# Performance work log

Measured on AMD Instinct MI355X. Metric: run time of the kernel, lower is better.

## Reference

```python
import math
import jax, jax.numpy as jnp
import numpy as np

DIM = 1024
HID = 2048  # dim * expansion_factor
QK = 128
G = 256  # group size
NUM_BUCKETS = 32
MAX_DIST = 128
SCALE = QK ** 0.5


def t5_rel_bias(rel_emb, g):
    # non-causal T5 relative position bias over a g x g window
    pos = jnp.arange(g)
    n = pos[:, None] - pos[None, :]  # n = -(k - q) = q - k
    nb = NUM_BUCKETS // 2  # 16
    ret = (n < 0).astype(jnp.int32) * nb
    n = jnp.abs(n)
    max_exact = nb // 2  # 8
    is_small = n < max_exact
    val_large = max_exact + (
        jnp.log(jnp.maximum(n, 1).astype(jnp.float32) / max_exact)
        / math.log(MAX_DIST / max_exact) * (nb - max_exact)
    ).astype(jnp.int32)
    val_large = jnp.minimum(val_large, nb - 1)
    bucket = ret + jnp.where(is_small, n, val_large)
    return rel_emb[bucket, 0] * SCALE  # [g, g]


def setup_inputs() -> dict:
    key = jax.random.key(0)
    ks = jax.random.split(key, 8)
    d = {}
    d['x'] = jax.random.normal(ks[0], (4, 4096, DIM), dtype=jnp.float32)
    d['ln_g'] = jnp.ones((DIM,), jnp.float32)
    d['ln_b'] = jnp.zeros((DIM,), jnp.float32)
    d['W_h'] = jax.random.normal(ks[1], (DIM, 2 * HID), jnp.float32) * (1.0 / math.sqrt(DIM))
    d['b_h'] = jnp.zeros((2 * HID,), jnp.float32)
    d['W_qk'] = jax.random.normal(ks[2], (DIM, QK), jnp.float32) * (1.0 / math.sqrt(DIM))
    d['b_qk'] = jnp.zeros((QK,), jnp.float32)
    d['os_g'] = 1.0 + 0.02 * jax.random.normal(ks[3], (4, QK), jnp.float32)
    d['os_b'] = jnp.zeros((4, QK), jnp.float32)
    d['rel_emb'] = jax.random.normal(ks[4], (NUM_BUCKETS, 1), jnp.float32)
    d['W_o'] = jax.random.normal(ks[5], (HID, DIM), jnp.float32) * (1.0 / math.sqrt(HID))
    d['b_o'] = jnp.zeros((DIM,), jnp.float32)
    return d


def reference(x, ln_g, ln_b, W_h, b_h, W_qk, b_qk, os_g, os_b, rel_emb, W_o, b_o):
    b, n, _ = x.shape
    # LayerNorm
    mu = jnp.mean(x, axis=-1, keepdims=True)
    var = jnp.var(x, axis=-1, keepdims=True)
    normed = (x - mu) * jax.lax.rsqrt(var + 1e-5) * ln_g + ln_b
    # to_hidden -> v, gate ; to_qk
    hidden = jax.nn.silu(normed @ W_h + b_h)  # [b, n, 2*HID]
    v, gate = hidden[..., :HID], hidden[..., HID:]
    qk = jax.nn.silu(normed @ W_qk + b_qk)  # [b, n, QK]
    # offset-scale into 4 heads
    heads = qk[..., None, :] * os_g + os_b  # [b, n, 4, QK]
    quad_q, lin_q, quad_k, lin_k = [heads[..., h, :] for h in range(4)]
    # group: n divisible by G (no padding needed)
    ng = n // G
    grp = lambda t: t.reshape(b, ng, G, -1)
    quad_q, quad_k, lin_q, lin_k, vg = map(grp, (quad_q, quad_k, lin_q, lin_k, v))
    # grouped quadratic attention with ReLU^2 and T5 bias
    sim = jnp.einsum('bgid,bgjd->bgij', quad_q, quad_k) / G
    sim = sim + t5_rel_bias(rel_emb, G)
    attn = jnp.square(jax.nn.relu(sim))
    quad_out = jnp.einsum('bgij,bgjd->bgid', attn, vg)
    # linear attention, reduced over groups (non-causal)
    lin_kv = jnp.einsum('bgnd,bgne->bde', lin_k, vg) / n
    lin_out = jnp.einsum('bgnd,bde->bgne', lin_q, lin_kv)
    out = gate * (quad_out.reshape(b, n, HID) + lin_out.reshape(b, n, HID))
    return out @ W_o + b_o + x
```

## Files before the change

### kernel.cpp

```cpp
#include <hip/hip_runtime.h>
#include <hip/hip_bf16.h>

typedef float  f32x4  __attribute__((ext_vector_type(4)));
typedef __bf16 bf16x8 __attribute__((ext_vector_type(8)));
typedef __bf16 bf16x4 __attribute__((ext_vector_type(4)));

__device__ __forceinline__ float silu_f(float x) { return x / (1.0f + __expf(-x)); }

__device__ __forceinline__ void gload16(const __bf16* g, const char* lds) {
    __builtin_amdgcn_global_load_lds((const __attribute__((address_space(1))) void*)g,
                                     (__attribute__((address_space(3))) void*)lds, 16, 0, 0);
}

__global__ __launch_bounds__(256) void ln_kernel(const float* __restrict__ x,
                                                 const float* __restrict__ g,
                                                 const float* __restrict__ b,
                                                 __bf16* __restrict__ out) {
    int row = blockIdx.x;
    const float* xr = x + (long)row * 1024;
    int t = threadIdx.x;
    f32x4 v = *(const f32x4*)(xr + t * 4);
    float s  = v[0] + v[1] + v[2] + v[3];
    float ss = v[0]*v[0] + v[1]*v[1] + v[2]*v[2] + v[3]*v[3];
    #pragma unroll
    for (int off = 32; off > 0; off >>= 1) {
        s  += __shfl_down(s, off);
        ss += __shfl_down(ss, off);
    }
    __shared__ float red[8];
    int wave = t >> 6, lane = t & 63;
    if (lane == 0) { red[wave*2] = s; red[wave*2+1] = ss; }
    __syncthreads();
    float S  = red[0] + red[2] + red[4] + red[6];
    float SS = red[1] + red[3] + red[5] + red[7];
    float mean = S * (1.0f/1024.0f);
    float var  = SS * (1.0f/1024.0f) - mean*mean;
    float rstd = rsqrtf(var + 1e-5f);
    __bf16* orow = out + (long)row * 1024;
    #pragma unroll
    for (int j = 0; j < 4; j++) {
        float fv = (v[j] - mean) * rstd * g[t*4+j] + b[t*4+j];
        orow[t*4+j] = (__bf16)fv;
    }
}

__global__ __launch_bounds__(256) void prep_kernel(const float* __restrict__ W_h,
                                                   const float* __restrict__ W_qk,
                                                   const float* __restrict__ W_o,
                                                   const float* __restrict__ rel_emb,
                                                   __bf16* __restrict__ WhT,
                                                   __bf16* __restrict__ WqkT,
                                                   __bf16* __restrict__ WoT,
                                                   float* __restrict__ bmat) {
    __shared__ __bf16 tile[32][33];
    int id = blockIdx.x, tid = threadIdx.x;
    if (id >= 6272) {
        int idx = (id - 6272) * 256 + tid;
        int i = idx >> 8, j = idx & 255;
        int n = i - j;
        int ret = (n < 0) ? 16 : 0;
        int an = (n < 0) ? -n : n;
        int bucket;
        if (an < 8) {
            bucket = ret + an;
        } else {
            float vl = logf((float)an * 0.125f) / 2.772588722239781f * 8.0f;
            int lv = 8 + (int)vl;
            bucket = ret + (lv < 15 ? lv : 15);
        }
        bmat[idx] = rel_emb[bucket] * 11.313708498984761f;
        return;
    }
    const float* in; __bf16* outp; int rows, cols, tx, ty;
    if (id < 4096)      { in = W_h;  outp = WhT;  rows = 1024; cols = 4096; tx = id % 128; ty = id / 128; }
    else if (id < 4224) { int t = id - 4096; in = W_qk; outp = WqkT; rows = 1024; cols = 128;  tx = t % 4;  ty = t / 4; }
    else                { int t = id - 4224; in = W_o;  outp = WoT;  rows = 2048; cols = 1024; tx = t % 32; ty = t / 32; }
    int c0 = tx * 32, r0 = ty * 32;
    int lx = tid & 31, ly = tid >> 5;
    #pragma unroll
    for (int i = 0; i < 4; i++) {
        int r = ly + i*8;
        tile[r][lx] = (__bf16)in[(long)(r0 + r) * cols + c0 + lx];
    }
    __syncthreads();
    #pragma unroll
    for (int i = 0; i < 4; i++) {
        int c = ly + i*8;
        outp[(long)(c0 + c) * rows + r0 + lx] = tile[lx][c];
    }
}

__global__ __launch_bounds__(256) void reduce8_kernel(const __bf16* __restrict__ in,
                                                      __bf16* __restrict__ out) {
    int i = (blockIdx.x * 256 + threadIdx.x) * 4;
    int b = i >> 18;
    int r = i & 262143;
    float s0 = 0.f, s1 = 0.f, s2 = 0.f, s3 = 0.f;
    #pragma unroll
    for (int c = 0; c < 8; ++c) {
        bf16x4 v = *(const bf16x4*)(in + ((long)(b*8 + c) << 18) + r);
        s0 += (float)v[0]; s1 += (float)v[1]; s2 += (float)v[2]; s3 += (float)v[3];
    }
    bf16x4 o; o[0] = (__bf16)s0; o[1] = (__bf16)s1; o[2] = (__bf16)s2; o[3] = (__bf16)s3;
    *(bf16x4*)(out + i) = o;
}

struct GP {
    const __bf16* A;
    const __bf16* B;
    const __bf16* A2;
    const __bf16* B2;
    int lda, ldb, kSteps;
    long sAz, sBz, sCz;
    float scale;
    float* outF;
    __bf16 *o0, *o1, *o2, *o3;
    const float *c0, *c1, *c2;
    __bf16* gbuf;
};

template<int EPI>
__global__ __launch_bounds__(256, 2) void gemm64_kernel(GP p) {
    __shared__ __bf16 As[2*128*32];
    __shared__ __bf16 Bs[2*128*32];
    const __bf16* A = p.A + (long)blockIdx.x * 128 * p.lda;
    const __bf16* B = p.B + (long)blockIdx.y * 128 * p.ldb;
    int tid = threadIdx.x;
    int wave = tid >> 6, lane = tid & 63;
    int wr = (wave >> 1) * 64, wc = (wave & 1) * 64;
    int lr = lane & 15, kg = lane >> 4;

    f32x4 acc[4][4] = {};

    int lsub = lane >> 2;
    int scol = (lane & 3) * 8;
    const __bf16* Ag = A + scol + (long)(wave*32 + lsub) * p.lda;
    const __bf16* Bg = B + scol + (long)(wave*32 + lsub) * p.ldb;
    long a16 = (long)16 * p.lda, b16 = (long)16 * p.ldb;
    __bf16* AsW = As + wave * 32 * 32;
    __bf16* BsW = Bs + wave * 32 * 32;

    for (int ks = 0; ks < p.kSteps; ++ks) {
        long k0 = (long)ks * 64;
        __syncthreads();
        gload16(Ag + k0,            (const char*)AsW);
        gload16(Ag + k0 + a16,      (const char*)(AsW + 16*32));
        gload16(Bg + k0,            (const char*)BsW);
        gload16(Bg + k0 + b16,      (const char*)(BsW + 16*32));
        gload16(Ag + k0 + 32,       (const char*)(AsW + 4096));
        gload16(Ag + k0 + 32 + a16, (const char*)(AsW + 4096 + 16*32));
        gload16(Bg + k0 + 32,       (const char*)(BsW + 4096));
        gload16(Bg + k0 + 32 + b16, (const char*)(BsW + 4096 + 16*32));
        __syncthreads();
#pragma unroll
        for (int kk = 0; kk < 2; ++kk) {
            bf16x8 af[4], bfr[4];
            #pragma unroll
            for (int i = 0; i < 4; i++) af[i]  = *(const bf16x8*)(As + kk*4096 + (wr + i*16 + lr)*32 + kg*8);
            #pragma unroll
            for (int i = 0; i < 4; i++) bfr[i] = *(const bf16x8*)(Bs + kk*4096 + (wc + i*16 + lr)*32 + kg*8);
            #pragma unroll
            for (int i = 0; i < 4; i++)
                #pragma unroll
                for (int j = 0; j < 4; j++)
                    acc[i][j] = __builtin_amdgcn_mfma_f32_16x16x32_bf16(af[i], bfr[j], acc[i][j], 0, 0, 0);
        }
    }

    int bx = blockIdx.x, by = blockIdx.y;
    #pragma unroll
    for (int i = 0; i < 4; i++) {
        #pragma unroll
        for (int j = 0; j < 4; j++) {
            int row0 = bx*128 + wr + i*16 + kg*4;
            int col  = by*128 + wc + j*16 + lr;
            if constexpr (EPI == 0) {
                if (col < 2048) {
                    bf16x4 vv;
                    #pragma unroll
                    for (int q = 0; q < 4; q++) vv[q] = (__bf16)silu_f(acc[i][j][q] + p.c0[col]);
                    *(bf16x4*)(p.o0 + (long)col*16384 + row0) = vv;
                } else {
                    #pragma unroll
                    for (int q = 0; q < 4; q++)
                        p.o1[(long)(row0+q)*2048 + (col - 2048)] = (__bf16)silu_f(acc[i][j][q] + p.c0[col]);
                }
            } else {
                #pragma unroll
                for (int q = 0; q < 4; q++) {
                    long idx = (long)(row0+q)*1024 + col;
                    p.outF[idx] = acc[i][j][q] + p.c0[col] + p.c1[idx];
                }
            }
        }
    }
}

template<int EPI>
__global__ __launch_bounds__(256, 2) void gemm_kernel(GP p) {
    __shared__ __bf16 As[128*32];
    __shared__ __bf16 Bs[128*32];
    int z = blockIdx.z;
    const __bf16* A = p.A + (long)z * p.sAz + (long)blockIdx.x * 128 * p.lda;
    const __bf16* B = p.B + (long)z * p.sBz + (long)blockIdx.y * 128 * p.ldb;
    int tid = threadIdx.x;
    int wave = tid >> 6, lane = tid & 63;
    int wr = (wave >> 1) * 64, wc = (wave & 1) * 64;
    int lr = lane & 15, kg = lane >> 4;

    f32x4 acc[4][4] = {};

    int lsub = lane >> 2;
    int scol = (lane & 3) * 8;
    const __bf16* Ag = A + scol + (long)(wave*32 + lsub) * p.lda;
    const __bf16* Bg = B + scol + (long)(wave*32 + lsub) * p.ldb;
    long a16 = (long)16 * p.lda, b16 = (long)16 * p.ldb;
    __bf16* AsW = As + wave * 32 * 32;
    __bf16* BsW = Bs + wave * 32 * 32;

    for (int ks = 0; ks < p.kSteps; ++ks) {
        long k0 = (long)ks * 32;
        __syncthreads();
        gload16(Ag + k0,       (const char*)AsW);
        gload16(Ag + k0 + a16, (const char*)(AsW + 16*32));
        gload16(Bg + k0,       (const char*)BsW);
        gload16(Bg + k0 + b16, (const char*)(BsW + 16*32));
        __syncthreads();
        bf16x8 af[4], bfr[4];
        #pragma unroll
        for (int i = 0; i < 4; i++) af[i]  = *(const bf16x8*)(As + (wr + i*16 + lr)*32 + kg*8);
        #pragma unroll
        for (int i = 0; i < 4; i++) bfr[i] = *(const bf16x8*)(Bs + (wc + i*16 + lr)*32 + kg*8);
        #pragma unroll
        for (int i = 0; i < 4; i++)
            #pragma unroll
            for (int j = 0; j < 4; j++)
                acc[i][j] = __builtin_amdgcn_mfma_f32_16x16x32_bf16(af[i], bfr[j], acc[i][j], 0, 0, 0);
    }

    int bx = blockIdx.x, by = blockIdx.y;
    #pragma unroll
    for (int i = 0; i < 4; i++) {
        #pragma unroll
        for (int j = 0; j < 4; j++) {
            int row0 = bx*128 + wr + i*16 + kg*4;
            int col  = by*128 + wc + j*16 + lr;
            if constexpr (EPI == 1) {
                float sv[4];
                #pragma unroll
                for (int q = 0; q < 4; q++) sv[q] = silu_f(acc[i][j][q] + p.c0[col]);
                #pragma unroll
                for (int q = 0; q < 4; q++) {
                    p.o0[(long)(row0+q)*128 + col] = (__bf16)(sv[q] * p.c1[      col] + p.c2[      col]);
                    p.o1[(long)(row0+q)*128 + col] = (__bf16)(sv[q] * p.c1[256 + col] + p.c2[256 + col]);
                    p.o2[(long)(row0+q)*128 + col] = (__bf16)(sv[q] * p.c1[128 + col] + p.c2[128 + col]);
                }
                bf16x4 lk;
                #pragma unroll
                for (int q = 0; q < 4; q++) lk[q] = (__bf16)(sv[q] * p.c1[384 + col] + p.c2[384 + col]);
                *(bf16x4*)(p.o3 + (long)col*16384 + row0) = lk;
            }
        }
    }
}

__global__ __launch_bounds__(256, 2) void simlinkv_kernel(GP ps, GP pl) {
    __shared__ __bf16 As[128*32];
    __shared__ __bf16 Bs[128*32];
    int id = blockIdx.x;
    bool sim = id < 256;
    GP p = sim ? ps : pl;
    int bx, by, z;
    if (sim) { bx = id & 1; by = (id >> 1) & 1; z = id >> 2; }
    else     { int t = id - 256; bx = 0; by = t & 15; z = t >> 4; }

    const __bf16* A = p.A + (long)z * p.sAz + (long)bx * 128 * p.lda;
    const __bf16* B = p.B + (long)z * p.sBz + (long)by * 128 * p.ldb;
    int tid = threadIdx.x;
    int wave = tid >> 6, lane = tid & 63;
    int wr = (wave >> 1) * 64, wc = (wave & 1) * 64;
    int lr = lane & 15, kg = lane >> 4;

    f32x4 acc[4][4] = {};

    int lsub = lane >> 2;
    int scol = (lane & 3) * 8;
    const __bf16* Ag = A + scol + (long)(wave*32 + lsub) * p.lda;
    const __bf16* Bg = B + scol + (long)(wave*32 + lsub) * p.ldb;
    long a16 = (long)16 * p.lda, b16 = (long)16 * p.ldb;
    __bf16* AsW = As + wave * 32 * 32;
    __bf16* BsW = Bs + wave * 32 * 32;

    for (int ks = 0; ks < p.kSteps; ++ks) {
        long k0 = (long)ks * 32;
        __syncthreads();
        gload16(Ag + k0,       (const char*)AsW);
        gload16(Ag + k0 + a16, (const char*)(AsW + 16*32));
        gload16(Bg + k0,       (const char*)BsW);
        gload16(Bg + k0 + b16, (const char*)(BsW + 16*32));
        __syncthreads();
        bf16x8 af[4], bfr[4];
        #pragma unroll
        for (int i = 0; i < 4; i++) af[i]  = *(const bf16x8*)(As + (wr + i*16 + lr)*32 + kg*8);
        #pragma unroll
        for (int i = 0; i < 4; i++) bfr[i] = *(const bf16x8*)(Bs + (wc + i*16 + lr)*32 + kg*8);
        #pragma unroll
        for (int i = 0; i < 4; i++)
            #pragma unroll
            for (int j = 0; j < 4; j++)
                acc[i][j] = __builtin_amdgcn_mfma_f32_16x16x32_bf16(af[i], bfr[j], acc[i][j], 0, 0, 0);
    }

    #pragma unroll
    for (int i = 0; i < 4; i++) {
        #pragma unroll
        for (int j = 0; j < 4; j++) {
            int row0 = bx*128 + wr + i*16 + kg*4;
            int col  = by*128 + wc + j*16 + lr;
            if (sim) {
                #pragma unroll
                for (int q = 0; q < 4; q++) {
                    int row = row0 + q;
                    float s = acc[i][j][q] * (1.0f/256.0f) + p.c0[row*256 + col];
                    s = fmaxf(s, 0.0f);
                    p.o0[(long)z*p.sCz + (long)row*256 + col] = (__bf16)(s * s);
                }
            } else {
                bf16x4 vv;
                #pragma unroll
                for (int q = 0; q < 4; q++) vv[q] = (__bf16)(acc[i][j][q] * p.scale);
                *(bf16x4*)(p.o0 + (long)z*p.sCz + (long)col*128 + row0) = vv;
            }
        }
    }
}

__global__ __launch_bounds__(256, 2) void quadlin_kernel(GP p) {
    __shared__ __bf16 As[128*32];
    __shared__ __bf16 Bs[128*32];
    int z = blockIdx.z;
    int batch = z >> 4;
    int tid = threadIdx.x;
    int wave = tid >> 6, lane = tid & 63;
    int wr = (wave >> 1) * 64, wc = (wave & 1) * 64;
    int lr = lane & 15, kg = lane >> 4;
    int lsub = lane >> 2;
    int scol = (lane & 3) * 8;
    __bf16* AsW = As + wave * 32 * 32;
    __bf16* BsW = Bs + wave * 32 * 32;

    f32x4 acc[4][4] = {};

    {
        const __bf16* Ag = p.A + (long)z * 65536 + (long)blockIdx.x * 128 * 256
                         + scol + (long)(wave*32 + lsub) * 256;
        const __bf16* Bg = p.B + (long)z * 256 + (long)blockIdx.y * 128 * 16384
                         + scol + (long)(wave*32 + lsub) * 16384;
        for (int ks = 0; ks < 8; ++ks) {
            long k0 = (long)ks * 32;
            __syncthreads();
            gload16(Ag + k0,             (const char*)AsW);
            gload16(Ag + k0 + 16*256,    (const char*)(AsW + 16*32));
            gload16(Bg + k0,             (const char*)BsW);
            gload16(Bg + k0 + 16L*16384, (const char*)(BsW + 16*32));
            __syncthreads();
            bf16x8 af[4], bfr[4];
            #pragma unroll
            for (int i = 0; i < 4; i++) af[i]  = *(const bf16x8*)(As + (wr + i*16 + lr)*32 + kg*8);
            #pragma unroll
            for (int i = 0; i < 4; i++) bfr[i] = *(const bf16x8*)(Bs + (wc + i*16 + lr)*32 + kg*8);
            #pragma unroll
            for (int i = 0; i < 4; i++)
                #pragma unroll
                for (int j = 0; j < 4; j++)
                    acc[i][j] = __builtin_amdgcn_mfma_f32_16x16x32_bf16(af[i], bfr[j], acc[i][j], 0, 0, 0);
        }
    }
    {
        const __bf16* Ag = p.A2 + ((long)z * 256 + (long)blockIdx.x * 128) * 128
                         + scol + (long)(wave*32 + lsub) * 128;
        const __bf16* Bg = p.B2 + (long)batch * 2048 * 128 + (long)blockIdx.y * 128 * 128
                         + scol + (long)(wave*32 + lsub) * 128;
        for (int ks = 0; ks < 4; ++ks) {
            long k0 = (long)ks * 32;
            __syncthreads();
            gload16(Ag + k0,          (const char*)AsW);
            gload16(Ag + k0 + 16*128, (const char*)(AsW + 16*32));
            gload16(Bg + k0,          (const char*)BsW);
            gload16(Bg + k0 + 16*128, (const char*)(BsW + 16*32));
            __syncthreads();
            bf16x8 af[4], bfr[4];
            #pragma unroll
            for (int i = 0; i < 4; i++) af[i]  = *(const bf16x8*)(As + (wr + i*16 + lr)*32 + kg*8);
            #pragma unroll
            for (int i = 0; i < 4; i++) bfr[i] = *(const bf16x8*)(Bs + (wc + i*16 + lr)*32 + kg*8);
            #pragma unroll
            for (int i = 0; i < 4; i++)
                #pragma unroll
                for (int j = 0; j < 4; j++)
                    acc[i][j] = __builtin_amdgcn_mfma_f32_16x16x32_bf16(af[i], bfr[j], acc[i][j], 0, 0, 0);
        }
    }
    #pragma unroll
    for (int i = 0; i < 4; i++) {
        #pragma unroll
        for (int j = 0; j < 4; j++) {
            int row0 = z*256 + blockIdx.x*128 + wr + i*16 + kg*4;
            int col  = blockIdx.y*128 + wc + j*16 + lr;
            #pragma unroll
            for (int q = 0; q < 4; q++) {
                long idx = (long)(row0+q)*2048 + col;
                float g = (float)p.gbuf[idx];
                p.gbuf[idx] = (__bf16)(g * acc[i][j][q]);
            }
        }
    }
}

extern "C" void kernel_launch(void* const* d_in, const int* in_sizes, int n_in,
                              void* d_out, int out_size, void* d_ws, size_t ws_size,
                              hipStream_t stream) {
    const float* x       = (const float*)d_in[0];
    const float* ln_g    = (const float*)d_in[1];
    const float* ln_b    = (const float*)d_in[2];
    const float* W_h     = (const float*)d_in[3];
    const float* b_h     = (const float*)d_in[4];
    const float* W_qk    = (const float*)d_in[5];
    const float* b_qk    = (const float*)d_in[6];
    const float* os_g    = (const float*)d_in[7];
    const float* os_b    = (const float*)d_in[8];
    const float* rel_emb = (const float*)d_in[9];
    const float* W_o     = (const float*)d_in[10];
    const float* b_o     = (const float*)d_in[11];
    float* out = (float*)d_out;

    const size_t MB = 1024 * 1024;
    if (ws_size < 190 * MB) return;

    char* ws = (char*)d_ws;
    __bf16* gate = (__bf16*)(ws + 0);
    __bf16* vT   = (__bf16*)(ws + 64*MB);
    __bf16* norm = (__bf16*)(ws + 128*MB);
    __bf16* attn = (__bf16*)(ws + 128*MB);
    __bf16* lkvT = (__bf16*)(ws + 136*MB);
    __bf16* lkvP = (__bf16*)(ws + 140*MB);
    __bf16* qq   = (__bf16*)(ws + 160*MB);
    __bf16* qk2  = (__bf16*)(ws + 164*MB);
    __bf16* lq   = (__bf16*)(ws + 168*MB);
    __bf16* lkT  = (__bf16*)(ws + 172*MB);
    float*  bmat = (float* )(ws + 176*MB);
    __bf16* WqkT = (__bf16*)(ws + 176*MB + 256*1024);
    __bf16* WoT  = (__bf16*)(ws + 177*MB);
    __bf16* WhT  = (__bf16*)(ws + 181*MB);

    prep_kernel<<<6528, 256, 0, stream>>>(W_h, W_qk, W_o, rel_emb, WhT, WqkT, WoT, bmat);
    ln_kernel<<<16384, 256, 0, stream>>>(x, ln_g, ln_b, norm);

    {
        GP p{}; p.A = norm; p.B = WhT; p.lda = 1024; p.ldb = 1024; p.kSteps = 16;
        p.c0 = b_h; p.o0 = vT; p.o1 = gate;
        gemm64_kernel<0><<<dim3(128, 32), 256, 0, stream>>>(p);
    }
    {
        GP p{}; p.A = norm; p.B = WqkT; p.lda = 1024; p.ldb = 1024; p.kSteps = 32;
        p.c0 = b_qk; p.c1 = os_g; p.c2 = os_b;
        p.o0 = qq; p.o1 = qk2; p.o2 = lq; p.o3 = lkT;
        gemm_kernel<1><<<dim3(128, 1, 1), 256, 0, stream>>>(p);
    }
    {
        GP ps{}; ps.A = qq; ps.B = qk2; ps.lda = 128; ps.ldb = 128; ps.kSteps = 4;
        ps.sAz = 256*128; ps.sBz = 256*128; ps.sCz = 256*256;
        ps.c0 = bmat; ps.o0 = attn;
        GP pl{}; pl.A = lkT; pl.B = vT; pl.lda = 16384; pl.ldb = 16384; pl.kSteps = 16;
        pl.sAz = 512; pl.sBz = 512; pl.sCz = 2048*128; pl.scale = 1.0f/4096.0f;
        pl.o0 = lkvP;
        simlinkv_kernel<<<768, 256, 0, stream>>>(ps, pl);
    }
    reduce8_kernel<<<1024, 256, 0, stream>>>(lkvP, lkvT);
    {
        GP p{}; p.A = attn; p.B = vT; p.A2 = lq; p.B2 = lkvT; p.gbuf = gate;
        quadlin_kernel<<<dim3(2, 16, 64), 256, 0, stream>>>(p);
    }
    {
        GP p{}; p.A = gate; p.B = WoT; p.lda = 2048; p.ldb = 2048; p.kSteps = 32;
        p.c0 = b_o; p.c1 = x; p.outF = out;
        gemm64_kernel<6><<<dim3(128, 8), 256, 0, stream>>>(p);
    }
}
```

Baseline: 433.6 us.

## Fuse prep with layernorm, merge qk GEMM into hidden GEMM, use K=64 steps

Merges the weight-prep and layernorm launches into one kernel by block-index ranges. The small qk projection, previously a 128-block GEMM, becomes an extra column tile (by==32) of the hidden-projection GEMM, so it runs alongside the big GEMM instead of as a separate underfilled launch. The sim/linkv and quad/lin kernels now load 64-wide K slices per barrier pair, halving the number of sync iterations at the cost of doubled LDS per block. Together these aim to cut launch count, tail underutilization and barrier overhead.

```diff
diff --git a/kernel.cpp b/kernel.cpp
--- a/kernel.cpp
+++ b/kernel.cpp
@@ -12,48 +12,48 @@
                                      (__attribute__((address_space(3))) void*)lds, 16, 0, 0);
 }
 
-__global__ __launch_bounds__(256) void ln_kernel(const float* __restrict__ x,
-                                                 const float* __restrict__ g,
-                                                 const float* __restrict__ b,
-                                                 __bf16* __restrict__ out) {
-    int row = blockIdx.x;
-    const float* xr = x + (long)row * 1024;
-    int t = threadIdx.x;
-    f32x4 v = *(const f32x4*)(xr + t * 4);
-    float s  = v[0] + v[1] + v[2] + v[3];
-    float ss = v[0]*v[0] + v[1]*v[1] + v[2]*v[2] + v[3]*v[3];
-    #pragma unroll
-    for (int off = 32; off > 0; off >>= 1) {
-        s  += __shfl_down(s, off);
-        ss += __shfl_down(ss, off);
-    }
+__global__ __launch_bounds__(256) void prepln_kernel(const float* __restrict__ x,
+                                                     const float* __restrict__ ln_g,
+                                                     const float* __restrict__ ln_b,
+                                                     __bf16* __restrict__ norm,
+                                                     const float* __restrict__ W_h,
+                                                     const float* __restrict__ W_qk,
+                                                     const float* __restrict__ W_o,
+                                                     const float* __restrict__ rel_emb,
+                                                     __bf16* __restrict__ WhT,
+                                                     __bf16* __restrict__ WqkT,
+                                                     __bf16* __restrict__ WoT,
+                                                     float* __restrict__ bmat) {
     __shared__ float red[8];
-    int wave = t >> 6, lane = t & 63;
-    if (lane == 0) { red[wave*2] = s; red[wave*2+1] = ss; }
-    __syncthreads();
-    float S  = red[0] + red[2] + red[4] + red[6];
-    float SS = red[1] + red[3] + red[5] + red[7];
-    float mean = S * (1.0f/1024.0f);
-    float var  = SS * (1.0f/1024.0f) - mean*mean;
-    float rstd = rsqrtf(var + 1e-5f);
-    __bf16* orow = out + (long)row * 1024;
-    #pragma unroll
-    for (int j = 0; j < 4; j++) {
-        float fv = (v[j] - mean) * rstd * g[t*4+j] + b[t*4+j];
-        orow[t*4+j] = (__bf16)fv;
-    }
-}
-
-__global__ __launch_bounds__(256) void prep_kernel(const float* __restrict__ W_h,
-                                                   const float* __restrict__ W_qk,
-                                                   const float* __restrict__ W_o,
-                                                   const float* __restrict__ rel_emb,
-                                                   __bf16* __restrict__ WhT,
-                                                   __bf16* __restrict__ WqkT,
-                                                   __bf16* __restrict__ WoT,
-                                                   float* __restrict__ bmat) {
     __shared__ __bf16 tile[32][33];
     int id = blockIdx.x, tid = threadIdx.x;
+    if (id < 16384) {
+        const float* xr = x + (long)id * 1024;
+        f32x4 v = *(const f32x4*)(xr + tid * 4);
+        float s  = v[0] + v[1] + v[2] + v[3];
+        float ss = v[0]*v[0] + v[1]*v[1] + v[2]*v[2] + v[3]*v[3];
+        #pragma unroll
+        for (int off = 32; off > 0; off >>= 1) {
+            s  += __shfl_down(s, off);
+            ss += __shfl_down(ss, off);
+        }
+        int wave = tid >> 6, lane = tid & 63;
+        if (lane == 0) { red[wave*2] = s; red[wave*2+1] = ss; }
+        __syncthreads();
+        float S  = red[0] + red[2] + red[4] + red[6];
+        float SS = red[1] + red[3] + red[5] + red[7];
+        float mean = S * (1.0f/1024.0f);
+        float var  = SS * (1.0f/1024.0f) - mean*mean;
+        float rstd = rsqrtf(var + 1e-5f);
+        __bf16* orow = norm + (long)id * 1024;
+        #pragma unroll
+        for (int j = 0; j < 4; j++) {
+            float fv = (v[j] - mean) * rstd * ln_g[tid*4+j] + ln_b[tid*4+j];
+            orow[tid*4+j] = (__bf16)fv;
+        }
+        return;
+    }
+    id -= 16384;
     if (id >= 6272) {
         int idx = (id - 6272) * 256 + tid;
         int i = idx >> 8, j = idx & 255;
@@ -114,17 +114,18 @@
     long sAz, sBz, sCz;
     float scale;
     float* outF;
-    __bf16 *o0, *o1, *o2, *o3;
-    const float *c0, *c1, *c2;
+    __bf16 *o0, *o1, *o2, *o3, *o4, *o5;
+    const float *c0, *c1, *c2, *c3;
     __bf16* gbuf;
 };
 
-template<int EPI>
-__global__ __launch_bounds__(256, 2) void gemm64_kernel(GP p) {
+__global__ __launch_bounds__(256, 2) void hqk_kernel(GP p) {
     __shared__ __bf16 As[2*128*32];
     __shared__ __bf16 Bs[2*128*32];
-    const __bf16* A = p.A + (long)blockIdx.x * 128 * p.lda;
-    const __bf16* B = p.B + (long)blockIdx.y * 128 * p.ldb;
+    int bx = blockIdx.x, by = blockIdx.y;
+    bool qkm = (by == 32);
+    const __bf16* A = p.A + (long)bx * 128 * 1024;
+    const __bf16* B = qkm ? p.B2 : p.B + (long)by * 128 * 1024;
     int tid = threadIdx.x;
     int wave = tid >> 6, lane = tid & 63;
     int wr = (wave >> 1) * 64, wc = (wave & 1) * 64;
@@ -134,23 +135,23 @@
 
     int lsub = lane >> 2;
     int scol = (lane & 3) * 8;
-    const __bf16* Ag = A + scol + (long)(wave*32 + lsub) * p.lda;
-    const __bf16* Bg = B + scol + (long)(wave*32 + lsub) * p.ldb;
-    long a16 = (long)16 * p.lda, b16 = (long)16 * p.ldb;
+    const __bf16* Ag = A + scol + (long)(wave*32 + lsub) * 1024;
+    const __bf16* Bg = B + scol + (long)(wave*32 + lsub) * 1024;
+    const long s16 = 16 * 1024;
     __bf16* AsW = As + wave * 32 * 32;
     __bf16* BsW = Bs + wave * 32 * 32;
 
-    for (int ks = 0; ks < p.kSteps; ++ks) {
+    for (int ks = 0; ks < 16; ++ks) {
         long k0 = (long)ks * 64;
         __syncthreads();
         gload16(Ag + k0,            (const char*)AsW);
-        gload16(Ag + k0 + a16,      (const char*)(AsW + 16*32));
+        gload16(Ag + k0 + s16,      (const char*)(AsW + 16*32));
         gload16(Bg + k0,            (const char*)BsW);
-        gload16(Bg + k0 + b16,      (const char*)(BsW + 16*32));
+        gload16(Bg + k0 + s16,      (const char*)(BsW + 16*32));
         gload16(Ag + k0 + 32,       (const char*)(AsW + 4096));
-        gload16(Ag + k0 + 32 + a16, (const char*)(AsW + 4096 + 16*32));
+        gload16(Ag + k0 + 32 + s16, (const char*)(AsW + 4096 + 16*32));
         gload16(Bg + k0 + 32,       (const char*)(BsW + 4096));
-        gload16(Bg + k0 + 32 + b16, (const char*)(BsW + 4096 + 16*32));
+        gload16(Bg + k0 + 32 + s16, (const char*)(BsW + 4096 + 16*32));
         __syncthreads();
 #pragma unroll
         for (int kk = 0; kk < 2; ++kk) {
@@ -167,14 +168,13 @@
         }
     }
 
-    int bx = blockIdx.x, by = blockIdx.y;
     #pragma unroll
     for (int i = 0; i < 4; i++) {
         #pragma unroll
         for (int j = 0; j < 4; j++) {
             int row0 = bx*128 + wr + i*16 + kg*4;
-            int col  = by*128 + wc + j*16 + lr;
-            if constexpr (EPI == 0) {
+            if (!qkm) {
+                int col = by*128 + wc + j*16 + lr;
                 if (col < 2048) {
                     bf16x4 vv;
                     #pragma unroll
@@ -186,23 +186,30 @@
                         p.o1[(long)(row0+q)*2048 + (col - 2048)] = (__bf16)silu_f(acc[i][j][q] + p.c0[col]);
                 }
             } else {
+                int col = wc + j*16 + lr;
+                float sv[4];
+                #pragma unroll
+                for (int q = 0; q < 4; q++) sv[q] = silu_f(acc[i][j][q] + p.c3[col]);
                 #pragma unroll
                 for (int q = 0; q < 4; q++) {
-                    long idx = (long)(row0+q)*1024 + col;
-                    p.outF[idx] = acc[i][j][q] + p.c0[col] + p.c1[idx];
+                    p.o2[(long)(row0+q)*128 + col] = (__bf16)(sv[q] * p.c1[      col] + p.c2[      col]);
+                    p.o3[(long)(row0+q)*128 + col] = (__bf16)(sv[q] * p.c1[256 + col] + p.c2[256 + col]);
+                    p.o4[(long)(row0+q)*128 + col] = (__bf16)(sv[q] * p.c1[128 + col] + p.c2[128 + col]);
                 }
+                bf16x4 lk;
+                #pragma unroll
+                for (int q = 0; q < 4; q++) lk[q] = (__bf16)(sv[q] * p.c1[384 + col] + p.c2[384 + col]);
+                *(bf16x4*)(p.o5 + (long)col*16384 + row0) = lk;
             }
         }
     }
 }
 
-template<int EPI>
-__global__ __launch_bounds__(256, 2) void gemm_kernel(GP p) {
-    __shared__ __bf16 As[128*32];
-    __shared__ __bf16 Bs[128*32];
-    int z = blockIdx.z;
-    const __bf16* A = p.A + (long)z * p.sAz + (long)blockIdx.x * 128 * p.lda;
-    const __bf16* B = p.B + (long)z * p.sBz + (long)blockIdx.y * 128 * p.ldb;
+__global__ __launch_bounds__(256, 2) void gemm64f_kernel(GP p) {
+    __shared__ __bf16 As[2*128*32];
+    __shared__ __bf16 Bs[2*128*32];
+    const __bf16* A = p.A + (long)blockIdx.x * 128 * p.lda;
+    const __bf16* B = p.B + (long)blockIdx.y * 128 * p.ldb;
     int tid = threadIdx.x;
     int wave = tid >> 6, lane = tid & 63;
     int wr = (wave >> 1) * 64, wc = (wave & 1) * 64;
@@ -219,23 +226,30 @@
     __bf16* BsW = Bs + wave * 32 * 32;
 
     for (int ks = 0; ks < p.kSteps; ++ks) {
-        long k0 = (long)ks * 32;
-        __syncthreads();
-        gload16(Ag + k0,       (const char*)AsW);
-        gload16(Ag + k0 + a16, (const char*)(AsW + 16*32));
-        gload16(Bg + k0,       (const char*)BsW);
-        gload16(Bg + k0 + b16, (const char*)(BsW + 16*32));
-        __syncthreads();
-        bf16x8 af[4], bfr[4];
-        #pragma unroll
-        for (int i = 0; i < 4; i++) af[i]  = *(const bf16x8*)(As + (wr + i*16 + lr)*32 + kg*8);
-        #pragma unroll
-        for (int i = 0; i < 4; i++) bfr[i] = *(const bf16x8*)(Bs + (wc + i*16 + lr)*32 + kg*8);
-        #pragma unroll
-        for (int i = 0; i < 4; i++)
-            #pragma unroll
-            for (int j = 0; j < 4; j++)
-                acc[i][j] = __builtin_amdgcn_mfma_f32_16x16x32_bf16(af[i], bfr[j], acc[i][j], 0, 0, 0);
+        long k0 = (long)ks * 64;
+        __syncthreads();
+        gload16(Ag + k0,            (const char*)AsW);
+        gload16(Ag + k0 + a16,      (const char*)(AsW + 16*32));
+        gload16(Bg + k0,            (const char*)BsW);
+        gload16(Bg + k0 + b16,      (const char*)(BsW + 16*32));
+        gload16(Ag + k0 + 32,       (const char*)(AsW + 4096));
+        gload16(Ag + k0 + 32 + a16, (const char*)(AsW + 4096 + 16*32));
+        gload16(Bg + k0 + 32,       (const char*)(BsW + 4096));
+        gload16(Bg + k0 + 32 + b16, (const char*)(BsW + 4096 + 16*32));
+        __syncthreads();
+#pragma unroll
+        for (int kk = 0; kk < 2; ++kk) {
+            bf16x8 af[4], bfr[4];
+            #pragma unroll
+            for (int i = 0; i < 4; i++) af[i]  = *(const bf16x8*)(As + kk*4096 + (wr + i*16 + lr)*32 + kg*8);
+            #pragma unroll
+            for (int i = 0; i < 4; i++) bfr[i] = *(const bf16x8*)(Bs + kk*4096 + (wc + i*16 + lr)*32 + kg*8);
+            #pragma unroll
+            for (int i = 0; i < 4; i++)
+                #pragma unroll
+                for (int j = 0; j < 4; j++)
+                    acc[i][j] = __builtin_amdgcn_mfma_f32_16x16x32_bf16(af[i], bfr[j], acc[i][j], 0, 0, 0);
+        }
     }
 
     int bx = blockIdx.x, by = blockIdx.y;
@@ -245,28 +259,18 @@
         for (int j = 0; j < 4; j++) {
             int row0 = bx*128 + wr + i*16 + kg*4;
             int col  = by*128 + wc + j*16 + lr;
-            if constexpr (EPI == 1) {
-                float sv[4];
-                #pragma unroll
-                for (int q = 0; q < 4; q++) sv[q] = silu_f(acc[i][j][q] + p.c0[col]);
-                #pragma unroll
-                for (int q = 0; q < 4; q++) {
-                    p.o0[(long)(row0+q)*128 + col] = (__bf16)(sv[q] * p.c1[      col] + p.c2[      col]);
-                    p.o1[(long)(row0+q)*128 + col] = (__bf16)(sv[q] * p.c1[256 + col] + p.c2[256 + col]);
-                    p.o2[(long)(row0+q)*128 + col] = (__bf16)(sv[q] * p.c1[128 + col] + p.c2[128 + col]);
-                }
-                bf16x4 lk;
-                #pragma unroll
-                for (int q = 0; q < 4; q++) lk[q] = (__bf16)(sv[q] * p.c1[384 + col] + p.c2[384 + col]);
-                *(bf16x4*)(p.o3 + (long)col*16384 + row0) = lk;
+            #pragma unroll
+            for (int q = 0; q < 4; q++) {
+                long idx = (long)(row0+q)*1024 + col;
+                p.outF[idx] = acc[i][j][q] + p.c0[col] + p.c1[idx];
             }
         }
     }
 }
 
 __global__ __launch_bounds__(256, 2) void simlinkv_kernel(GP ps, GP pl) {
-    __shared__ __bf16 As[128*32];
-    __shared__ __bf16 Bs[128*32];
+    __shared__ __bf16 As[2*128*32];
+    __shared__ __bf16 Bs[2*128*32];
     int id = blockIdx.x;
     bool sim = id < 256;
     GP p = sim ? ps : pl;
@@ -292,23 +296,30 @@
     __bf16* BsW = Bs + wave * 32 * 32;
 
     for (int ks = 0; ks < p.kSteps; ++ks) {
-        long k0 = (long)ks * 32;
-        __syncthreads();
-        gload16(Ag + k0,       (const char*)AsW);
-        gload16(Ag + k0 + a16, (const char*)(AsW + 16*32));
-        gload16(Bg + k0,       (const char*)BsW);
-        gload16(Bg + k0 + b16, (const char*)(BsW + 16*32));
-        __syncthreads();
-        bf16x8 af[4], bfr[4];
-        #pragma unroll
-        for (int i = 0; i < 4; i++) af[i]  = *(const bf16x8*)(As + (wr + i*16 + lr)*32 + kg*8);
-        #pragma unroll
-        for (int i = 0; i < 4; i++) bfr[i] = *(const bf16x8*)(Bs + (wc + i*16 + lr)*32 + kg*8);
-        #pragma unroll
-        for (int i = 0; i < 4; i++)
-            #pragma unroll
-            for (int j = 0; j < 4; j++)
-                acc[i][j] = __builtin_amdgcn_mfma_f32_16x16x32_bf16(af[i], bfr[j], acc[i][j], 0, 0, 0);
+        long k0 = (long)ks * 64;
+        __syncthreads();
+        gload16(Ag + k0,            (const char*)AsW);
+        gload16(Ag + k0 + a16,      (const char*)(AsW + 16*32));
+        gload16(Bg + k0,            (const char*)BsW);
+        gload16(Bg + k0 + b16,      (const char*)(BsW + 16*32));
+        gload16(Ag + k0 + 32,       (const char*)(AsW + 4096));
+        gload16(Ag + k0 + 32 + a16, (const char*)(AsW + 4096 + 16*32));
+        gload16(Bg + k0 + 32,       (const char*)(BsW + 4096));
+        gload16(Bg + k0 + 32 + b16, (const char*)(BsW + 4096 + 16*32));
+        __syncthreads();
+#pragma unroll
+        for (int kk = 0; kk < 2; ++kk) {
+            bf16x8 af[4], bfr[4];
+            #pragma unroll
+            for (int i = 0; i < 4; i++) af[i]  = *(const bf16x8*)(As + kk*4096 + (wr + i*16 + lr)*32 + kg*8);
+            #pragma unroll
+            for (int i = 0; i < 4; i++) bfr[i] = *(const bf16x8*)(Bs + kk*4096 + (wc + i*16 + lr)*32 + kg*8);
+            #pragma unroll
+            for (int i = 0; i < 4; i++)
+                #pragma unroll
+                for (int j = 0; j < 4; j++)
+                    acc[i][j] = __builtin_amdgcn_mfma_f32_16x16x32_bf16(af[i], bfr[j], acc[i][j], 0, 0, 0);
+        }
     }
 
     #pragma unroll
@@ -336,8 +347,8 @@
 }
 
 __global__ __launch_bounds__(256, 2) void quadlin_kernel(GP p) {
-    __shared__ __bf16 As[128*32];
-    __shared__ __bf16 Bs[128*32];
+    __shared__ __bf16 As[2*128*32];
+    __shared__ __bf16 Bs[2*128*32];
     int z = blockIdx.z;
     int batch = z >> 4;
     int tid = threadIdx.x;
@@ -356,24 +367,32 @@
                          + scol + (long)(wave*32 + lsub) * 256;
         const __bf16* Bg = p.B + (long)z * 256 + (long)blockIdx.y * 128 * 16384
                          + scol + (long)(wave*32 + lsub) * 16384;
-        for (int ks = 0; ks < 8; ++ks) {
-            long k0 = (long)ks * 32;
+        const long a16 = 16*256, b16 = 16L*16384;
+        for (int ks = 0; ks < 4; ++ks) {
+            long k0 = (long)ks * 64;
             __syncthreads();
-            gload16(Ag + k0,             (const char*)AsW);
-            gload16(Ag + k0 + 16*256,    (const char*)(AsW + 16*32));
-            gload16(Bg + k0,             (const char*)BsW);
-            gload16(Bg + k0 + 16L*16384, (const char*)(BsW + 16*32));
+            gload16(Ag + k0,            (const char*)AsW);
+            gload16(Ag + k0 + a16,      (const char*)(AsW + 16*32));
+            gload16(Bg + k0,            (const char*)BsW);
+            gload16(Bg + k0 + b16,      (const char*)(BsW + 16*32));
+            gload16(Ag + k0 + 32,       (const char*)(AsW + 4096));
+            gload16(Ag + k0 + 32 + a16, (const char*)(AsW + 4096 + 16*32));
+            gload16(Bg + k0 + 32,       (const char*)(BsW + 4096));
+            gload16(Bg + k0 + 32 + b16, (const char*)(BsW + 4096 + 16*32));
             __syncthreads();
-            bf16x8 af[4], bfr[4];
-            #pragma unroll
-            for (int i = 0; i < 4; i++) af[i]  = *(const bf16x8*)(As + (wr + i*16 + lr)*32 + kg*8);
-            #pragma unroll
-            for (int i = 0; i < 4; i++) bfr[i] = *(const bf16x8*)(Bs + (wc + i*16 + lr)*32 + kg*8);
-            #pragma unroll
-            for (int i = 0; i < 4; i++)
-                #pragma unroll
-                for (int j = 0; j < 4; j++)
-                    acc[i][j] = __builtin_amdgcn_mfma_f32_16x16x32_bf16(af[i], bfr[j], acc[i][j], 0, 0, 0);
+#pragma unroll
+            for (int kk = 0; kk < 2; ++kk) {
+                bf16x8 af[4], bfr[4];
+                #pragma unroll
+                for (int i = 0; i < 4; i++) af[i]  = *(const bf16x8*)(As + kk*4096 + (wr + i*16 + lr)*32 + kg*8);
+                #pragma unroll
+                for (int i = 0; i < 4; i++) bfr[i] = *(const bf16x8*)(Bs + kk*4096 + (wc + i*16 + lr)*32 + kg*8);
+                #pragma unroll
+                for (int i = 0; i < 4; i++)
+                    #pragma unroll
+                    for (int j = 0; j < 4; j++)
+                        acc[i][j] = __builtin_amdgcn_mfma_f32_16x16x32_bf16(af[i], bfr[j], acc[i][j], 0, 0, 0);
+            }
         }
     }
     {
@@ -381,24 +400,32 @@
                          + scol + (long)(wave*32 + lsub) * 128;
         const __bf16* Bg = p.B2 + (long)batch * 2048 * 128 + (long)blockIdx.y * 128 * 128
                          + scol + (long)(wave*32 + lsub) * 128;
-        for (int ks = 0; ks < 4; ++ks) {
-            long k0 = (long)ks * 32;
+        const long a16 = 16*128, b16 = 16*128;
+        for (int ks = 0; ks < 2; ++ks) {
+            long k0 = (long)ks * 64;
             __syncthreads();
-            gload16(Ag + k0,          (const char*)AsW);
-            gload16(Ag + k0 + 16*128, (const char*)(AsW + 16*32));
-            gload16(Bg + k0,          (const char*)BsW);
-            gload16(Bg + k0 + 16*128, (const char*)(BsW + 16*32));
+            gload16(Ag + k0,            (const char*)AsW);
+            gload16(Ag + k0 + a16,      (const char*)(AsW + 16*32));
+            gload16(Bg + k0,            (const char*)BsW);
+            gload16(Bg + k0 + b16,      (const char*)(BsW + 16*32));
+            gload16(Ag + k0 + 32,       (const char*)(AsW + 4096));
+            gload16(Ag + k0 + 32 + a16, (const char*)(AsW + 4096 + 16*32));
+            gload16(Bg + k0 + 32,       (const char*)(BsW + 4096));
+            gload16(Bg + k0 + 32 + b16, (const char*)(BsW + 4096 + 16*32));
             __syncthreads();
-            bf16x8 af[4], bfr[4];
-            #pragma unroll
-            for (int i = 0; i < 4; i++) af[i]  = *(const bf16x8*)(As + (wr + i*16 + lr)*32 + kg*8);
-            #pragma unroll
-            for (int i = 0; i < 4; i++) bfr[i] = *(const bf16x8*)(Bs + (wc + i*16 + lr)*32 + kg*8);
-            #pragma unroll
-            for (int i = 0; i < 4; i++)
-                #pragma unroll
-                for (int j = 0; j < 4; j++)
-                    acc[i][j] = __builtin_amdgcn_mfma_f32_16x16x32_bf16(af[i], bfr[j], acc[i][j], 0, 0, 0);
+#pragma unroll
+            for (int kk = 0; kk < 2; ++kk) {
+                bf16x8 af[4], bfr[4];
+                #pragma unroll
+                for (int i = 0; i < 4; i++) af[i]  = *(const bf16x8*)(As + kk*4096 + (wr + i*16 + lr)*32 + kg*8);
+                #pragma unroll
+                for (int i = 0; i < 4; i++) bfr[i] = *(const bf16x8*)(Bs + kk*4096 + (wc + i*16 + lr)*32 + kg*8);
+                #pragma unroll
+                for (int i = 0; i < 4; i++)
+                    #pragma unroll
+                    for (int j = 0; j < 4; j++)
+                        acc[i][j] = __builtin_amdgcn_mfma_f32_16x16x32_bf16(af[i], bfr[j], acc[i][j], 0, 0, 0);
+            }
         }
     }
     #pragma unroll
@@ -453,25 +480,22 @@
     __bf16* WoT  = (__bf16*)(ws + 177*MB);
     __bf16* WhT  = (__bf16*)(ws + 181*MB);
 
-    prep_kernel<<<6528, 256, 0, stream>>>(W_h, W_qk, W_o, rel_emb, WhT, WqkT, WoT, bmat);
-    ln_kernel<<<16384, 256, 0, stream>>>(x, ln_g, ln_b, norm);
+    prepln_kernel<<<22912, 256, 0, stream>>>(x, ln_g, ln_b, norm,
+                                             W_h, W_qk, W_o, rel_emb,
+                                             WhT, WqkT, WoT, bmat);
 
     {
-        GP p{}; p.A = norm; p.B = WhT; p.lda = 1024; p.ldb = 1024; p.kSteps = 16;
+        GP p{}; p.A = norm; p.B = WhT; p.B2 = WqkT;
         p.c0 = b_h; p.o0 = vT; p.o1 = gate;
-        gemm64_kernel<0><<<dim3(128, 32), 256, 0, stream>>>(p);
+        p.c3 = b_qk; p.c1 = os_g; p.c2 = os_b;
+        p.o2 = qq; p.o3 = qk2; p.o4 = lq; p.o5 = lkT;
+        hqk_kernel<<<dim3(128, 33), 256, 0, stream>>>(p);
     }
     {
-        GP p{}; p.A = norm; p.B = WqkT; p.lda = 1024; p.ldb = 1024; p.kSteps = 32;
-        p.c0 = b_qk; p.c1 = os_g; p.c2 = os_b;
-        p.o0 = qq; p.o1 = qk2; p.o2 = lq; p.o3 = lkT;
-        gemm_kernel<1><<<dim3(128, 1, 1), 256, 0, stream>>>(p);
-    }
-    {
-        GP ps{}; ps.A = qq; ps.B = qk2; ps.lda = 128; ps.ldb = 128; ps.kSteps = 4;
+        GP ps{}; ps.A = qq; ps.B = qk2; ps.lda = 128; ps.ldb = 128; ps.kSteps = 2;
         ps.sAz = 256*128; ps.sBz = 256*128; ps.sCz = 256*256;
         ps.c0 = bmat; ps.o0 = attn;
-        GP pl{}; pl.A = lkT; pl.B = vT; pl.lda = 16384; pl.ldb = 16384; pl.kSteps = 16;
+        GP pl{}; pl.A = lkT; pl.B = vT; pl.lda = 16384; pl.ldb = 16384; pl.kSteps = 8;
         pl.sAz = 512; pl.sBz = 512; pl.sCz = 2048*128; pl.scale = 1.0f/4096.0f;
         pl.o0 = lkvP;
         simlinkv_kernel<<<768, 256, 0, stream>>>(ps, pl);
@@ -484,6 +508,6 @@
     {
         GP p{}; p.A = gate; p.B = WoT; p.lda = 2048; p.ldb = 2048; p.kSteps = 32;
         p.c0 = b_o; p.c1 = x; p.outF = out;
-        gemm64_kernel<6><<<dim3(128, 8), 256, 0, stream>>>(p);
-    }
-}
+        gemm64f_kernel<<<dim3(128, 8), 256, 0, stream>>>(p);
+    }
+}
```

Measured after the change: 412.1 us. 5.0% less time.
